# Performance work log

Measured on AMD Instinct MI355X. Metric: run time of the kernel, lower is better.

## Reference

```python
import jax, jax.numpy as jnp
import numpy as np

T, B, D, H, P = 256, 256, 128, 512, 3  # time, batch, covariate_dim, hidden_dim, n_dist_params (ggd)


def setup_inputs() -> dict:
    key = jax.random.key(0)
    ks = jax.random.split(key, 12)
    return {
        "x": jax.random.normal(ks[0], (T, B, D + 1), jnp.float32),          # time-major padded covariates, col 0 = time
        "h0": jax.random.normal(ks[1], (B, H), jnp.float32),                 # random initial hidden (as in torch forward)
        "lengths": jax.random.randint(ks[2], (B,), 2, T + 1),                # valid sequence lengths, >= 2
        "w_ih": jax.random.normal(ks[3], (3 * H, D + 1), jnp.float32) * 0.02,
        "w_hh": jax.random.normal(ks[4], (3 * H, H), jnp.float32) * 0.02,
        "b_ih": jnp.zeros((3 * H,), jnp.float32),
        "b_hh": jnp.zeros((3 * H,), jnp.float32),
        "w1": jax.random.normal(ks[5], (10 * D, H + 1), jnp.float32) * 0.02,  # cov_fc_layer1
        "b1": jnp.zeros((10 * D,), jnp.float32),
        "w2": jax.random.normal(ks[6], (D, 10 * D), jnp.float32) * 0.02,      # cov_fc_layer2
        "b2": jnp.zeros((D,), jnp.float32),
        "wp": jax.random.normal(ks[7], (P, H), jnp.float32) * 0.001,          # params_fc_layer (xavier gain=0.001)
        "bp": jax.random.normal(ks[8], (P,), jnp.float32) * 1e-5,
    }


def _gru(x, h0, lengths, w_ih, w_hh, b_ih, b_hh):
    # Packed-sequence GRU: freeze hidden state past each sequence's length
    # (so h_last matches torch's last_hidden_state) and zero-pad outputs
    # (matching pad_packed_sequence).
    xw = jnp.einsum('tbd,gd->tbg', x, w_ih) + b_ih  # [T,B,3H] gate precompute
    tvec = jnp.arange(x.shape[0])

    def step(h, inputs):
        xw_t, t = inputs
        hw = h @ w_hh.T + b_hh
        xr, xz, xn = jnp.split(xw_t, 3, axis=-1)
        hr, hz, hn = jnp.split(hw, 3, axis=-1)
        r = jax.nn.sigmoid(xr + hr)
        z = jax.nn.sigmoid(xz + hz)
        n = jnp.tanh(xn + r * hn)
        h_new = (1.0 - z) * n + z * h
        valid = (t < lengths)[:, None]
        return jnp.where(valid, h_new, h), jnp.where(valid, h_new, 0.0)

    h_last, outs = jax.lax.scan(step, h0, (xw, tvec))
    return outs, h_last  # outs: [T,B,H], h_last: [B,H]


def _forward(x, h0, lengths, w_ih, w_hh, b_ih, b_hh, w1, b1, w2, b2, wp, bp):
    outs, h_last = _gru(x, h0, lengths, w_ih, w_hh, b_ih, b_hh)
    hidden = outs.transpose(1, 0, 2)          # [B,T,H]
    covs = x.transpose(1, 0, 2)               # [B,T,D+1]
    # time_deltas[b,i] = time[b,i+1] - time[b,i] (0 appended at end)
    times = covs[:, :, 0]
    td = jnp.concatenate([times[:, 1:], jnp.zeros((times.shape[0], 1), times.dtype)], axis=1) - times
    hwt = jnp.concatenate([hidden, td[:, :, None]], axis=2)  # [B,T,H+1]
    # Batched version of the per-(batch,timestep) tiny MLP loop, steps 0..T-2
    pre = jax.nn.sigmoid(jnp.einsum('bth,kh->btk', hwt[:, :-1], w1) + b1)  # [B,T-1,10D]
    preds = jnp.einsum('btk,dk->btd', pre, w2) + b2                         # [B,T-1,D]
    step_idx = jnp.arange(preds.shape[1])
    mask = (step_idx[None, :] < (lengths - 1)[:, None])[:, :, None]
    preds = jnp.where(mask, preds, 0.0)
    # distribution parameters from last hidden state; all ggd params positive -> exp(-x)
    dist_params = jnp.exp(-(h_last @ wp.T + bp))  # [B,P]
    return preds, dist_params


def reference(x, h0, lengths, w_ih, w_hh, b_ih, b_hh, w1, b1, w2, b2, wp, bp):
    preds, dist_params = _forward(x, h0, lengths, w_ih, w_hh, b_ih, b_hh, w1, b1, w2, b2, wp, bp)
    return preds, dist_params, lengths
```

## Files before the change

### kernel.cpp

```cpp
#include <hip/hip_runtime.h>
#include <hip/hip_bf16.h>
#include <math.h>

#define TT 256
#define BB 256
#define DP1 129
#define HH 512
#define K1 1280
#define DD 128
#define RTOT 65280
#define XKP 144
#define HKP 528

#define U_X16   0
#define U_WHF   9437184
#define U_WXF   10248192
#define U_H0    10469376
#define U_BAR   10604544
#define U_W1P   10604800
#define U_W2P   11280640
#define U_HIST  11444480
#define U_FLAGS 46047488
#define PREP_N  12494080
#define OUT_DIST 8355840
#define OUT_LEN  8356608

typedef __attribute__((ext_vector_type(8))) short bf16x8;
typedef __attribute__((ext_vector_type(16))) float f32x16;

__device__ __forceinline__ float sigm(float v) { return 1.0f / (1.0f + __expf(-v)); }

__device__ __forceinline__ unsigned short bfbits(float f) {
    union { __hip_bfloat16 h; unsigned short u; } cv;
    cv.h = __float2bfloat16(f);
    return cv.u;
}

__global__ __launch_bounds__(256) void prep_kernel(
    const float* __restrict__ x, const float* __restrict__ h0,
    const float* __restrict__ w_ih, const float* __restrict__ w_hh,
    const float* __restrict__ b_ih, const float* __restrict__ b_hh,
    const float* __restrict__ w1, const float* __restrict__ b1,
    const float* __restrict__ w2,
    __hip_bfloat16* __restrict__ bf)
{
    int i = blockIdx.x * 256 + threadIdx.x;
    if (i < 9437184) {
        int tb = i / XKP, k = i - tb * XKP;
        float v = (k < DP1) ? x[(size_t)tb * DP1 + k] : (k == DP1 ? 1.0f : 0.0f);
        bf[U_X16 + i] = __float2bfloat16(v);
    } else if (i < 10248192) {
        int r = i - 9437184;
        int e = r & 7;
        int lane = (r >> 3) & 63;
        int rem = r >> 9;
        int kc = rem % 33, gi = rem / 33;
        int jb = gi / 3, g = gi - jb * 3;
        int j = jb * 32 + (lane & 31);
        int k = kc * 16 + (lane >> 5) * 8 + e;
        float v = (k < HH) ? w_hh[(size_t)(g * HH + j) * HH + k]
                : (k == HH ? b_hh[g * HH + j] : 0.0f);
        bf[U_WHF + r] = __float2bfloat16(v);
    } else if (i < 10469376) {
        int r = i - 10248192;
        int e = r & 7;
        int lane = (r >> 3) & 63;
        int rem = r >> 9;
        int kc = rem % 9, gi = rem / 9;
        int jb = gi / 3, g = gi - jb * 3;
        int j = jb * 32 + (lane & 31);
        int k = kc * 16 + (lane >> 5) * 8 + e;
        float v = (k < DP1) ? w_ih[(size_t)(g * HH + j) * DP1 + k]
                : (k == DP1 ? b_ih[g * HH + j] : 0.0f);
        bf[U_WXF + r] = __float2bfloat16(v);
    } else if (i < 10604544) {
        int r = i - 10469376;
        int b = r / HKP, k = r - b * HKP;
        float v = (k < HH) ? h0[(size_t)b * HH + k] : (k == HH ? 1.0f : 0.0f);
        bf[U_H0 + r] = __float2bfloat16(v);
    } else if (i < 10604800) {
        bf[U_BAR + (i - 10604544)] = __float2bfloat16(0.0f);
    } else if (i < 11280640) {
        int r = i - 10604800;
        int e = r & 7;
        int lane = (r >> 3) & 63;
        int rem = r >> 9;
        int kc = rem % 33, tile = rem / 33;
        int col = tile * 32 + (lane & 31);
        int k = kc * 16 + (lane >> 5) * 8 + e;
        float v = (k < HH) ? w1[(size_t)col * 513 + k]
                : (k == HH ? b1[col]
                : (k == HH + 1 ? w1[(size_t)col * 513 + 512] : 0.0f));
        bf[U_W1P + r] = __float2bfloat16(v);
    } else if (i < 11444480) {
        int r = i - 11280640;
        int e = r & 7;
        int lane = (r >> 3) & 63;
        int rem = r >> 9;
        int kc = rem % 80, tile = rem / 80;
        int col = tile * 32 + (lane & 31);
        int k = kc * 16 + (lane >> 5) * 8 + e;
        bf[U_W2P + r] = __float2bfloat16(w2[(size_t)col * K1 + k]);
    } else if (i < 12493056) {
        int idx = i - 11444480;
        int row = idx >> 4, c = idx & 15;
        bf[U_HIST + (size_t)row * HKP + HH + c] =
            __float2bfloat16(c == 0 ? 1.0f : 0.0f);
    } else if (i < PREP_N) {
        int idx = i - 12493056;
        if (idx < 512) ((int*)(bf + U_FLAGS))[idx] = 0;
    }
}

__global__ __launch_bounds__(256, 1) void gru_scan(
    const __hip_bfloat16* __restrict__ x16,
    const __hip_bfloat16* __restrict__ h0p,
    __hip_bfloat16* __restrict__ hist,
    const __hip_bfloat16* __restrict__ whf,
    const __hip_bfloat16* __restrict__ wxf,
    const int* __restrict__ lengths,
    int* __restrict__ flags,
    int* __restrict__ nego)
{
    __shared__ float p[4][32][33];
    __shared__ int fastS;
    const int tid  = threadIdx.x;
    const int bt   = blockIdx.x;
    const int jblk = blockIdx.y;
    const int b0   = bt * 32;
    const int wid  = tid >> 6;
    const int ln   = tid & 63;
    const int row  = b0 + (ln & 31);
    const int khi  = (ln >> 5) * 8;
    int* myflag = flags + bt * 64 + jblk;

    if (tid == 0) {
        int xcc = 0;
        asm volatile("s_getreg_b32 %0, hwreg(HW_REG_XCC_ID, 0, 32)" : "=s"(xcc));
        atomicOr(nego + bt, 1 << (xcc & 7));
        __threadfence();
        atomicAdd(nego + 8 + bt, 1);
        while (__hip_atomic_load(nego + 8 + bt, __ATOMIC_RELAXED,
                                 __HIP_MEMORY_SCOPE_AGENT) < 16)
            __builtin_amdgcn_s_sleep(1);
        int m = __hip_atomic_load(nego + bt, __ATOMIC_RELAXED,
                                  __HIP_MEMORY_SCOPE_AGENT);
        fastS = (__popc((unsigned)m) == 1);
    }
    __syncthreads();
    const bool fast = (fastS != 0);

    bf16x8 bh[33], bx[9];
    if (wid < 3) {
        const bf16x8* bH = (const bf16x8*)whf + ((jblk * 3 + wid) * 33) * 64 + ln;
        #pragma unroll
        for (int kc = 0; kc < 33; ++kc) bh[kc] = bH[kc * 64];
        const bf16x8* bX = (const bf16x8*)wxf + ((jblk * 3 + wid) * 9) * 64 + ln;
        #pragma unroll
        for (int kc = 0; kc < 9; ++kc) bx[kc] = bX[kc * 64];
    }

    const int br = tid >> 3;
    const int lenb = lengths[b0 + br];
    float hreg[2][2];
    #pragma unroll
    for (int i = 0; i < 2; ++i) {
        int gj = jblk * 32 + 2 * ((tid & 7) + 8 * i);
        hreg[i][0] = __bfloat162float(h0p[(size_t)(b0 + br) * HKP + gj]);
        hreg[i][1] = __bfloat162float(h0p[(size_t)(b0 + br) * HKP + gj + 1]);
    }

    bf16x8 ax[9];
    f32x16 accX = {};
    if (wid < 3) {
        const bf16x8* aX = (const bf16x8*)(x16 + (size_t)row * XKP + khi);
        #pragma unroll
        for (int kc = 0; kc < 9; ++kc) ax[kc] = aX[kc * 2];
        #pragma unroll
        for (int kc = 0; kc < 9; ++kc)
            accX = __builtin_amdgcn_mfma_f32_32x32x16_bf16(ax[kc], bx[kc], accX, 0, 0, 0);
    }

    for (int t = 0; t < TT; ++t) {
        const __hip_bfloat16* hprev = (t == 0) ? h0p : (hist + (size_t)(t - 1) * BB * HKP);
        __hip_bfloat16* hout = hist + (size_t)t * BB * HKP;

        if (wid < 3) {
            f32x16 accHa = {}, accHb = {};
            const bf16x8* aH = (const bf16x8*)(hprev + (size_t)row * HKP + khi);
            #pragma unroll
            for (int kc = 0; kc < 32; kc += 2) {
                accHa = __builtin_amdgcn_mfma_f32_32x32x16_bf16(aH[kc * 2], bh[kc], accHa, 0, 0, 0);
                accHb = __builtin_amdgcn_mfma_f32_32x32x16_bf16(aH[(kc + 1) * 2], bh[kc + 1], accHb, 0, 0, 0);
            }
            accHa = __builtin_amdgcn_mfma_f32_32x32x16_bf16(aH[32 * 2], bh[32], accHa, 0, 0, 0);

            const int col = ln & 31;
            const int rh = 4 * (ln >> 5);
            if (wid < 2) {
                f32x16 s = accHa + accHb + accX;
                #pragma unroll
                for (int r = 0; r < 16; ++r)
                    p[wid][(r & 3) + 8 * (r >> 2) + rh][col] = s[r];
            } else {
                f32x16 sh = accHa + accHb;
                #pragma unroll
                for (int r = 0; r < 16; ++r) {
                    int rr = (r & 3) + 8 * (r >> 2) + rh;
                    p[2][rr][col] = accX[r];
                    p[3][rr][col] = sh[r];
                }
            }
        }
        __syncthreads();

        {
            const bool valid = (t < lenb);
            #pragma unroll
            for (int i = 0; i < 2; ++i) {
                int j0 = 2 * ((tid & 7) + 8 * i);
                float rr0 = sigm(p[0][br][j0]);
                float zz0 = sigm(p[1][br][j0]);
                float nn0 = tanhf(p[2][br][j0] + rr0 * p[3][br][j0]);
                float h0v = valid ? ((1.f - zz0) * nn0 + zz0 * hreg[i][0]) : hreg[i][0];
                float rr1 = sigm(p[0][br][j0 + 1]);
                float zz1 = sigm(p[1][br][j0 + 1]);
                float nn1 = tanhf(p[2][br][j0 + 1] + rr1 * p[3][br][j0 + 1]);
                float h1v = valid ? ((1.f - zz1) * nn1 + zz1 * hreg[i][1]) : hreg[i][1];
                hreg[i][0] = h0v;
                hreg[i][1] = h1v;
                unsigned uv = (unsigned)bfbits(h0v) | ((unsigned)bfbits(h1v) << 16);
                *(unsigned*)(hout + (size_t)(b0 + br) * HKP + jblk * 32 + j0) = uv;
            }
        }
        __syncthreads();

        if (t < TT - 1) {
            if (tid == 0) {
                if (!fast) __threadfence();
                __hip_atomic_store(myflag, t + 1, __ATOMIC_RELAXED, __HIP_MEMORY_SCOPE_AGENT);
            }
            if (wid < 3) {
                const bf16x8* aX = (const bf16x8*)(x16 + ((size_t)(t + 1) * BB + row) * XKP + khi);
                #pragma unroll
                for (int kc = 0; kc < 9; ++kc) ax[kc] = aX[kc * 2];
                f32x16 aXn = {};
                #pragma unroll
                for (int kc = 0; kc < 9; ++kc)
                    aXn = __builtin_amdgcn_mfma_f32_32x32x16_bf16(ax[kc], bx[kc], aXn, 0, 0, 0);
                accX = aXn;
            }
            if (wid == 3) {
                const int* f = flags + bt * 64 + (ln & 15);
                while (true) {
                    int v = __hip_atomic_load(f, __ATOMIC_RELAXED, __HIP_MEMORY_SCOPE_AGENT);
                    if (__all(v >= t + 1)) break;
                    __builtin_amdgcn_s_sleep(1);
                }
                if (!fast) __threadfence();
            }
            __syncthreads();
        }
    }
}

__global__ __launch_bounds__(256) void td_kernel(
    const float* __restrict__ x, __hip_bfloat16* __restrict__ hist)
{
    int r = blockIdx.x * 256 + threadIdx.x;
    if (r < RTOT) {
        int b = r / 255, t = r - b * 255;
        float td = x[((size_t)(t + 1) * BB + b) * DP1] - x[((size_t)t * BB + b) * DP1];
        hist[((size_t)t * BB + b) * HKP + 513] = __float2bfloat16(td);
    }
}

__global__ __launch_bounds__(256) void head_mfma(
    const __hip_bfloat16* __restrict__ hist,
    const __hip_bfloat16* __restrict__ w1p,
    const __hip_bfloat16* __restrict__ w2p,
    const float* __restrict__ b2,
    const int* __restrict__ lengths,
    float* __restrict__ out)
{
    __shared__ __hip_bfloat16 preS[64 * 264];
    const int tid = threadIdx.x;
    const int wv  = tid >> 6;
    const int ln  = tid & 63;
    const int r0  = blockIdx.x * 64;
    const int m   = ln & 31;
    const int khi = (ln >> 5) * 8;

    const __hip_bfloat16* aBase0;
    const __hip_bfloat16* aBase1;
    {
        int r = r0 + m;
        int b = r / 255, t = r - b * 255;
        aBase0 = hist + ((size_t)t * BB + b) * HKP + khi;
        r = r0 + 32 + m;
        b = r / 255; t = r - b * 255;
        aBase1 = hist + ((size_t)t * BB + b) * HKP + khi;
    }

    f32x16 acc20 = {}, acc21 = {};

    for (int c = 0; c < 5; ++c) {
        f32x16 s00 = {}, s01 = {}, s10 = {}, s11 = {};
        const int t0 = c * 8 + wv * 2;
        const bf16x8* bp0 = (const bf16x8*)w1p + ((size_t)t0 * 33) * 64 + ln;
        const bf16x8* bp1 = bp0 + 33 * 64;
        #pragma unroll 4
        for (int kc = 0; kc < 33; ++kc) {
            bf16x8 a0 = *(const bf16x8*)(aBase0 + kc * 16);
            bf16x8 a1 = *(const bf16x8*)(aBase1 + kc * 16);
            bf16x8 w0 = bp0[kc * 64];
            bf16x8 w1f = bp1[kc * 64];
            s00 = __builtin_amdgcn_mfma_f32_32x32x16_bf16(a0, w0, s00, 0, 0, 0);
            s01 = __builtin_amdgcn_mfma_f32_32x32x16_bf16(a0, w1f, s01, 0, 0, 0);
            s10 = __builtin_amdgcn_mfma_f32_32x32x16_bf16(a1, w0, s10, 0, 0, 0);
            s11 = __builtin_amdgcn_mfma_f32_32x32x16_bf16(a1, w1f, s11, 0, 0, 0);
        }
        const int colL = wv * 64 + m;
        const int rb = 4 * (ln >> 5);
        #pragma unroll
        for (int reg = 0; reg < 16; ++reg) {
            int rr = (reg & 3) + 8 * (reg >> 2) + rb;
            preS[rr * 264 + colL]             = __float2bfloat16(sigm(s00[reg]));
            preS[rr * 264 + colL + 32]        = __float2bfloat16(sigm(s01[reg]));
            preS[(rr + 32) * 264 + colL]      = __float2bfloat16(sigm(s10[reg]));
            preS[(rr + 32) * 264 + colL + 32] = __float2bfloat16(sigm(s11[reg]));
        }
        __syncthreads();

        const bf16x8* b2p = (const bf16x8*)w2p + ((size_t)wv * 80 + c * 16) * 64 + ln;
        #pragma unroll 4
        for (int j = 0; j < 16; ++j) {
            bf16x8 pa0 = *(const bf16x8*)(preS + m * 264 + j * 16 + khi);
            bf16x8 pa1 = *(const bf16x8*)(preS + (32 + m) * 264 + j * 16 + khi);
            bf16x8 wb = b2p[j * 64];
            acc20 = __builtin_amdgcn_mfma_f32_32x32x16_bf16(pa0, wb, acc20, 0, 0, 0);
            acc21 = __builtin_amdgcn_mfma_f32_32x32x16_bf16(pa1, wb, acc21, 0, 0, 0);
        }
        __syncthreads();
    }

    const int d = wv * 32 + m;
    const float bias = b2[d];
    const int rb = 4 * (ln >> 5);
    #pragma unroll
    for (int reg = 0; reg < 16; ++reg) {
        int rr = (reg & 3) + 8 * (reg >> 2) + rb;
        {
            int r = r0 + rr;
            int b = r / 255, t = r - b * 255;
            bool valid = t < (lengths[b] - 1);
            out[(size_t)r * DD + d] = valid ? (acc20[reg] + bias) : 0.f;
        }
        {
            int r = r0 + 32 + rr;
            int b = r / 255, t = r - b * 255;
            bool valid = t < (lengths[b] - 1);
            out[(size_t)r * DD + d] = valid ? (acc21[reg] + bias) : 0.f;
        }
    }
}

__global__ __launch_bounds__(256) void tail_kernel(
    const __hip_bfloat16* __restrict__ hist,
    const float* __restrict__ wp,
    const float* __restrict__ bp,
    const int* __restrict__ lengths,
    float* __restrict__ out)
{
    int gid = blockIdx.x * 256 + threadIdx.x;
    if (gid < 768) {
        int b = gid / 3, pidx = gid - b * 3;
        float acc = bp[pidx];
        const __hip_bfloat16* hr = hist + ((size_t)(TT - 1) * BB + b) * HKP;
        const float* wr = wp + (size_t)pidx * HH;
        #pragma unroll 4
        for (int k = 0; k < HH; ++k) acc += __bfloat162float(hr[k]) * wr[k];
        out[OUT_DIST + gid] = __expf(-acc);
    } else if (gid < 1024) {
        int b = gid - 768;
        out[OUT_LEN + b] = (float)lengths[b];
    }
}

extern "C" void kernel_launch(void* const* d_in, const int* in_sizes, int n_in,
                              void* d_out, int out_size, void* d_ws, size_t ws_size,
                              hipStream_t stream)
{
    const float* x       = (const float*)d_in[0];
    const float* h0      = (const float*)d_in[1];
    const int*   lengths = (const int*)d_in[2];
    const float* w_ih    = (const float*)d_in[3];
    const float* w_hh    = (const float*)d_in[4];
    const float* b_ih    = (const float*)d_in[5];
    const float* b_hh    = (const float*)d_in[6];
    const float* w1      = (const float*)d_in[7];
    const float* b1      = (const float*)d_in[8];
    const float* w2      = (const float*)d_in[9];
    const float* b2      = (const float*)d_in[10];
    const float* wp      = (const float*)d_in[11];
    const float* bp      = (const float*)d_in[12];
    float* out = (float*)d_out;

    __hip_bfloat16* bf   = (__hip_bfloat16*)d_ws;
    __hip_bfloat16* x16  = bf + U_X16;
    __hip_bfloat16* whf  = bf + U_WHF;
    __hip_bfloat16* wxf  = bf + U_WXF;
    __hip_bfloat16* h16i = bf + U_H0;
    __hip_bfloat16* w1p  = bf + U_W1P;
    __hip_bfloat16* w2p  = bf + U_W2P;
    __hip_bfloat16* hist = bf + U_HIST;
    int* flags           = (int*)(bf + U_FLAGS);
    int* nego            = (int*)(bf + U_BAR);

    prep_kernel<<<PREP_N / 256, 256, 0, stream>>>(
        x, h0, w_ih, w_hh, b_ih, b_hh, w1, b1, w2, bf);

    gru_scan<<<dim3(8, 16), 256, 0, stream>>>(x16, h16i, hist, whf, wxf, lengths,
                                              flags, nego);

    td_kernel<<<(RTOT + 255) / 256, 256, 0, stream>>>(x, hist);

    head_mfma<<<RTOT / 64, 256, 0, stream>>>(hist, w1p, w2p, b2, lengths, out);

    tail_kernel<<<4, 256, 0, stream>>>(hist, wp, bp, lengths, out);
}
```

Measured before the change: 2.146 ms.

## Poll step flags in compute waves, drop barrier, use raw asm flag ops

```diff
diff --git a/kernel.cpp b/kernel.cpp
--- a/kernel.cpp
+++ b/kernel.cpp
@@ -29,6 +29,12 @@
 typedef __attribute__((ext_vector_type(16))) float f32x16;
 
 __device__ __forceinline__ float sigm(float v) { return 1.0f / (1.0f + __expf(-v)); }
+
+__device__ __forceinline__ float tanhfast(float x) {
+    x = fminf(20.f, fmaxf(-20.f, x));
+    float e = __expf(2.f * x);
+    return (e - 1.f) / (e + 1.f);
+}
 
 __device__ __forceinline__ unsigned short bfbits(float f) {
     union { __hip_bfloat16 h; unsigned short u; } cv;
@@ -221,11 +227,11 @@
                 int j0 = 2 * ((tid & 7) + 8 * i);
                 float rr0 = sigm(p[0][br][j0]);
                 float zz0 = sigm(p[1][br][j0]);
-                float nn0 = tanhf(p[2][br][j0] + rr0 * p[3][br][j0]);
+                float nn0 = tanhfast(p[2][br][j0] + rr0 * p[3][br][j0]);
                 float h0v = valid ? ((1.f - zz0) * nn0 + zz0 * hreg[i][0]) : hreg[i][0];
                 float rr1 = sigm(p[0][br][j0 + 1]);
                 float zz1 = sigm(p[1][br][j0 + 1]);
-                float nn1 = tanhf(p[2][br][j0 + 1] + rr1 * p[3][br][j0 + 1]);
+                float nn1 = tanhfast(p[2][br][j0 + 1] + rr1 * p[3][br][j0 + 1]);
                 float h1v = valid ? ((1.f - zz1) * nn1 + zz1 * hreg[i][1]) : hreg[i][1];
                 hreg[i][0] = h0v;
                 hreg[i][1] = h1v;
@@ -237,8 +243,15 @@
 
         if (t < TT - 1) {
             if (tid == 0) {
-                if (!fast) __threadfence();
-                __hip_atomic_store(myflag, t + 1, __ATOMIC_RELAXED, __HIP_MEMORY_SCOPE_AGENT);
+                if (fast) {
+                    int tv = t + 1;
+                    asm volatile("global_store_dword %0, %1, off"
+                                 :: "v"(myflag), "v"(tv) : "memory");
+                } else {
+                    __threadfence();
+                    __hip_atomic_store(myflag, t + 1, __ATOMIC_RELAXED,
+                                       __HIP_MEMORY_SCOPE_AGENT);
+                }
             }
             if (wid < 3) {
                 const bf16x8* aX = (const bf16x8*)(x16 + ((size_t)(t + 1) * BB + row) * XKP + khi);
@@ -249,17 +262,27 @@
                 for (int kc = 0; kc < 9; ++kc)
                     aXn = __builtin_amdgcn_mfma_f32_32x32x16_bf16(ax[kc], bx[kc], aXn, 0, 0, 0);
                 accX = aXn;
+
+                const int* f = flags + bt * 64 + (ln & 15);
+                if (fast) {
+                    while (true) {
+                        int v;
+                        asm volatile("global_load_dword %0, %1, off sc0\n\t"
+                                     "s_waitcnt vmcnt(0)"
+                                     : "=v"(v) : "v"(f) : "memory");
+                        if (__all(v >= t + 1)) break;
+                        __builtin_amdgcn_s_sleep(1);
+                    }
+                } else {
+                    while (true) {
+                        int v = __hip_atomic_load(f, __ATOMIC_RELAXED,
+                                                  __HIP_MEMORY_SCOPE_AGENT);
+                        if (__all(v >= t + 1)) break;
+                        __builtin_amdgcn_s_sleep(1);
+                    }
+                    __threadfence();
+                }
             }
-            if (wid == 3) {
-                const int* f = flags + bt * 64 + (ln & 15);
-                while (true) {
-                    int v = __hip_atomic_load(f, __ATOMIC_RELAXED, __HIP_MEMORY_SCOPE_AGENT);
-                    if (__all(v >= t + 1)) break;
-                    __builtin_amdgcn_s_sleep(1);
-                }
-                if (!fast) __threadfence();
-            }
-            __syncthreads();
         }
     }
 }
```

Result: faster. 1.958 ms (-8.8%).
